# Kernel tuning notes

Hardware: AMD Instinct MI355X
Metric: run time of the kernel (lower is better)

The kernel has to match this reference:

```python
import jax, jax.numpy as jnp
import numpy as np

SHIFT_HZ = 20.0
SAMPLE_RATE = 16000
N_FFT = 512
SHIFT_BINS = SHIFT_HZ / (SAMPLE_RATE / N_FFT)  # 0.64 bins
EPS = 1e-08


def setup_inputs() -> dict:
    key = jax.random.key(0)
    # log-magnitude spectrogram [B, 1, F, T]
    x = jax.random.normal(key, (32, 1, 257, 4096), dtype=jnp.float32)
    return {"x": x}


def reference(x):
    B, C, F, T = x.shape
    x_lin = jnp.power(10.0, x[:, 0])  # [B, F, T] linear magnitude

    f = jnp.arange(F, dtype=jnp.float32)
    target = f + SHIFT_BINS                     # source bin (fractional)
    f_low = jnp.floor(target)
    f_high = jnp.ceil(target)
    alpha = (target - f_low).astype(x.dtype)    # interp weight; 0 when integer

    valid = (target >= 0) & (target < F) & (f_low < F) & (f_high < F)
    lo = jnp.clip(f_low.astype(jnp.int32), 0, F - 1)
    hi = jnp.clip(f_high.astype(jnp.int32), 0, F - 1)

    # gather along frequency axis + linear interp (alpha==0 reduces to copy)
    interp = ((1.0 - alpha)[None, :, None] * jnp.take(x_lin, lo, axis=1)
              + alpha[None, :, None] * jnp.take(x_lin, hi, axis=1))
    shifted = jnp.where(valid[None, :, None], interp, 0.0)

    return jnp.log10(shifted + EPS)[:, None]    # [B, 1, F, T]
```

## Files before the change

### kernel.cpp

```cpp
#include <hip/hip_runtime.h>

#define B_DIM 32
#define F_DIM 257
#define T_DIM 4096
#define EPS_F 1e-8f

#define LOG2_10  3.32192809488736234787f
#define LOG10_2  0.30102999566398119521f

#define NBLK      (B_DIM * F_DIM)
#define XCD_CHUNK (NBLK / 8)

typedef float f32x4 __attribute__((ext_vector_type(4)));

__device__ __forceinline__ float pow10_fast(float v) {
    return __builtin_amdgcn_exp2f(v * LOG2_10);
}
__device__ __forceinline__ float log10_fast(float v) {
    return __builtin_amdgcn_logf(v) * LOG10_2;
}

__global__ __launch_bounds__(256) void freq_shift_kernel(
        const float* __restrict__ x, float* __restrict__ out) {
    const int bid = blockIdx.x;
    const int bf  = (bid & 7) * XCD_CHUNK + (bid >> 3);

    const int f  = bf % F_DIM;
    const long long base = (long long)bf * T_DIM;
    const int tid = threadIdx.x;

    f32x4* __restrict__ orow = (f32x4*)(out + base);

    if (f == F_DIM - 1) {
        const float cv = log10_fast(EPS_F);
        f32x4 v; v.x = cv; v.y = cv; v.z = cv; v.w = cv;
#pragma unroll
        for (int i = 0; i < T_DIM / 4 / 256; ++i)
            __builtin_nontemporal_store(v, orow + i * 256 + tid);
        return;
    }

    const f32x4* __restrict__ row0 = (const f32x4*)(x + base);
    const f32x4* __restrict__ row1 = (const f32x4*)(x + base + T_DIM);

    const float ff     = (float)f;
    const float target = ff + 0.64f;
    const float alpha  = target - ff;
    const float beta   = 1.0f - alpha;

    f32x4 va[4], vb[4];
#pragma unroll
    for (int i = 0; i < 4; ++i) {
        va[i] = row0[i * 256 + tid];
        vb[i] = row1[i * 256 + tid];
    }
    __builtin_amdgcn_sched_barrier(0);

#pragma unroll
    for (int i = 0; i < 4; ++i) {
        f32x4 r;
        r.x = log10_fast(beta * pow10_fast(va[i].x) + alpha * pow10_fast(vb[i].x) + EPS_F);
        r.y = log10_fast(beta * pow10_fast(va[i].y) + alpha * pow10_fast(vb[i].y) + EPS_F);
        r.z = log10_fast(beta * pow10_fast(va[i].z) + alpha * pow10_fast(vb[i].z) + EPS_F);
        r.w = log10_fast(beta * pow10_fast(va[i].w) + alpha * pow10_fast(vb[i].w) + EPS_F);
        __builtin_nontemporal_store(r, orow + i * 256 + tid);
    }
}

extern "C" void kernel_launch(void* const* d_in, const int* in_sizes, int n_in,
                              void* d_out, int out_size, void* d_ws, size_t ws_size,
                              hipStream_t stream) {
    const float* x = (const float*)d_in[0];
    float* out = (float*)d_out;
    dim3 grid(NBLK);
    dim3 block(256);
    freq_shift_kernel<<<grid, block, 0, stream>>>(x, out);
}
```

Measured before the change: 235.4 us.

## Process frequency bands per block with LDS-staged async row pipeline

Each block now handles a 16-row frequency band for one batch instead of a single output row. Input rows are streamed into a 4-slot LDS ring with global_load_lds, prefetching two rows ahead. The pow10 of the previous row is kept in registers so every input row is read from global memory and exponentiated once rather than twice. This halves redundant global reads and transcendental work, but leaves far fewer blocks (512) and lower occupancy because of the 64KB LDS buffer, with a block barrier per row.

```diff
diff --git a/kernel.cpp b/kernel.cpp
--- a/kernel.cpp
+++ b/kernel.cpp
@@ -8,10 +8,14 @@
 #define LOG2_10  3.32192809488736234787f
 #define LOG10_2  0.30102999566398119521f
 
-#define NBLK      (B_DIM * F_DIM)
-#define XCD_CHUNK (NBLK / 8)
+#define BAND   16
+#define NBANDS 16
+#define NBLK   (B_DIM * NBANDS)
+#define SLOTS  4
 
 typedef float f32x4 __attribute__((ext_vector_type(4)));
+typedef __attribute__((address_space(1))) void* gvoidp;
+typedef __attribute__((address_space(3))) void* svoidp;
 
 __device__ __forceinline__ float pow10_fast(float v) {
     return __builtin_amdgcn_exp2f(v * LOG2_10);
@@ -22,48 +26,86 @@
 
 __global__ __launch_bounds__(256) void freq_shift_kernel(
         const float* __restrict__ x, float* __restrict__ out) {
+    __shared__ float lds[SLOTS][T_DIM];
+
     const int bid = blockIdx.x;
-    const int bf  = (bid & 7) * XCD_CHUNK + (bid >> 3);
+    const int id  = (bid & 7) * (NBLK / 8) + (bid >> 3);
+    const int b   = id >> 4;
+    const int fb  = id & (NBANDS - 1);
+    const int f0  = fb * BAND;
+    const int tid = threadIdx.x;
+    const int wid = tid >> 6;
 
-    const int f  = bf % F_DIM;
-    const long long base = (long long)bf * T_DIM;
-    const int tid = threadIdx.x;
+    const float* __restrict__ xb = x   + ((long long)(b * F_DIM + f0)) * T_DIM;
+    float* __restrict__       ob = out + ((long long)(b * F_DIM + f0)) * T_DIM;
 
-    f32x4* __restrict__ orow = (f32x4*)(out + base);
+    auto stage = [&](int k) {
+        const float* src = xb + (long long)k * T_DIM + (tid << 2);
+#pragma unroll
+        for (int j = 0; j < 4; ++j) {
+            float* dst = &lds[k & 3][j * 1024 + wid * 256];
+            __builtin_amdgcn_global_load_lds((gvoidp)(src + j * 1024),
+                                             (svoidp)dst, 16, 0, 0);
+        }
+    };
 
-    if (f == F_DIM - 1) {
-        const float cv = log10_fast(EPS_F);
-        f32x4 v; v.x = cv; v.y = cv; v.z = cv; v.w = cv;
+    stage(0);
+    stage(1);
+    asm volatile("s_waitcnt vmcnt(4)" ::: "memory");
+    __builtin_amdgcn_sched_barrier(0);
+    __builtin_amdgcn_s_barrier();
+
+    f32x4 p[4];
+    {
+        const f32x4* s0 = (const f32x4*)&lds[0][0];
 #pragma unroll
-        for (int i = 0; i < T_DIM / 4 / 256; ++i)
-            __builtin_nontemporal_store(v, orow + i * 256 + tid);
-        return;
+        for (int j = 0; j < 4; ++j) {
+            const f32x4 v = s0[j * 256 + tid];
+            p[j].x = pow10_fast(v.x); p[j].y = pow10_fast(v.y);
+            p[j].z = pow10_fast(v.z); p[j].w = pow10_fast(v.w);
+        }
     }
 
-    const f32x4* __restrict__ row0 = (const f32x4*)(x + base);
-    const f32x4* __restrict__ row1 = (const f32x4*)(x + base + T_DIM);
+#pragma unroll
+    for (int r = 0; r < BAND; ++r) {
+        if (r + 2 <= BAND) {
+            stage(r + 2);
+            asm volatile("s_waitcnt vmcnt(4)" ::: "memory");
+        } else {
+            asm volatile("s_waitcnt vmcnt(0)" ::: "memory");
+        }
+        __builtin_amdgcn_sched_barrier(0);
+        __builtin_amdgcn_s_barrier();
 
-    const float ff     = (float)f;
-    const float target = ff + 0.64f;
-    const float alpha  = target - ff;
-    const float beta   = 1.0f - alpha;
+        const float ff    = (float)(f0 + r);
+        const float alpha = (ff + 0.64f) - ff;
+        const float beta  = 1.0f - alpha;
 
-    f32x4 va[4], vb[4];
+        const f32x4* sn = (const f32x4*)&lds[(r + 1) & 3][0];
+        f32x4* orow = (f32x4*)(ob + (long long)r * T_DIM);
 #pragma unroll
-    for (int i = 0; i < 4; ++i) {
-        va[i] = row0[i * 256 + tid];
-        vb[i] = row1[i * 256 + tid];
+        for (int j = 0; j < 4; ++j) {
+            const f32x4 v = sn[j * 256 + tid];
+            f32x4 pn;
+            pn.x = pow10_fast(v.x); pn.y = pow10_fast(v.y);
+            pn.z = pow10_fast(v.z); pn.w = pow10_fast(v.w);
+            f32x4 res;
+            res.x = log10_fast(beta * p[j].x + alpha * pn.x + EPS_F);
+            res.y = log10_fast(beta * p[j].y + alpha * pn.y + EPS_F);
+            res.z = log10_fast(beta * p[j].z + alpha * pn.z + EPS_F);
+            res.w = log10_fast(beta * p[j].w + alpha * pn.w + EPS_F);
+            __builtin_nontemporal_store(res, orow + j * 256 + tid);
+            p[j] = pn;
+        }
     }
-    __builtin_amdgcn_sched_barrier(0);
 
+    if (fb == NBANDS - 1) {
+        const float cv = log10_fast(EPS_F);
+        f32x4 vv; vv.x = cv; vv.y = cv; vv.z = cv; vv.w = cv;
+        f32x4* orow = (f32x4*)(ob + (long long)BAND * T_DIM);
 #pragma unroll
-    for (int i = 0; i < 4; ++i) {
-        f32x4 r;
-        r.x = log10_fast(beta * pow10_fast(va[i].x) + alpha * pow10_fast(vb[i].x) + EPS_F);
-        r.y = log10_fast(beta * pow10_fast(va[i].y) + alpha * pow10_fast(vb[i].y) + EPS_F);
-        r.z = log10_fast(beta * pow10_fast(va[i].z) + alpha * pow10_fast(vb[i].z) + EPS_F);
-        r.w = log10_fast(beta * pow10_fast(va[i].w) + alpha * pow10_fast(vb[i].w) + EPS_F);
-        __builtin_nontemporal_store(r, orow + i * 256 + tid);
+        for (int j = 0; j < 4; ++j)
+            __builtin_nontemporal_store(vv, orow + j * 256 + tid);
     }
 }
 
```

New measurement: 238.9 us. About the same (+1.5%).
